# Performance work log

Hardware: AMD Instinct MI355X
Metric: run time of the kernel (lower is better)

## Reference

```python
import jax, jax.numpy as jnp
import numpy as np

N_HEADS = 16
N_KV_HEADS = 4
D_HEAD = 128
LN_EPS = 1e-5


def _layernorm_nobias(x, gamma):
    # LayerNorm over last dim, elementwise affine weight only (bias=False)
    mu = jnp.mean(x, axis=-1, keepdims=True)
    var = jnp.mean(jnp.square(x - mu), axis=-1, keepdims=True)
    return (x - mu) * jax.lax.rsqrt(var + LN_EPS) * gamma


def setup_inputs() -> dict:
    key = jax.random.key(0)
    ks = jax.random.split(key, 7)
    B, T, C = 1, 2048, 2048
    s = 1.0 / np.sqrt(C)
    return {
        "x": jax.random.normal(ks[0], (B, T, C), dtype=jnp.float32),
        "Wq": jax.random.normal(ks[1], (C, C), dtype=jnp.float32) * s,
        "Wk": jax.random.normal(ks[2], (C, N_KV_HEADS * D_HEAD), dtype=jnp.float32) * s,
        "Wv": jax.random.normal(ks[3], (C, N_KV_HEADS * D_HEAD), dtype=jnp.float32) * s,
        "Wo": jax.random.normal(ks[4], (C, C), dtype=jnp.float32) * s,
        "gq": jnp.ones((D_HEAD,), dtype=jnp.float32),
        "gk": jnp.ones((D_HEAD,), dtype=jnp.float32),
        "temp": jnp.asarray(np.log(10.0), dtype=jnp.float32),
    }


def reference(x, Wq, Wk, Wv, Wo, gq, gk, temp):
    B, T, C = x.shape
    g = N_HEADS // N_KV_HEADS
    q = (x @ Wq).reshape(B, T, N_HEADS, D_HEAD)
    k = (x @ Wk).reshape(B, T, N_KV_HEADS, D_HEAD)
    v = (x @ Wv).reshape(B, T, N_KV_HEADS, D_HEAD)
    # GQA: repeat_interleave kv heads along head dim
    k = jnp.repeat(k, g, axis=2)
    v = jnp.repeat(v, g, axis=2)
    q = _layernorm_nobias(q, gq)
    k = _layernorm_nobias(k, gk)
    scale = jnp.minimum(jnp.exp(temp), 50.0)
    scores = jnp.einsum('bthd,bshd->bhts', q, k) * scale  # [B,H,T,T]
    causal = jnp.tril(jnp.ones((T, T), dtype=bool))       # True = keep
    scores = jnp.where(causal[None, None], scores, -jnp.inf)
    attn = jax.nn.softmax(scores, axis=-1)
    out = jnp.einsum('bhts,bshd->bthd', attn, v).reshape(B, T, C)
    return out @ Wo
```

## Files before the change

### kernel.cpp

```cpp
#include <hip/hip_runtime.h>
#include <stdint.h>

typedef unsigned short u16;
typedef __bf16 bf16x8 __attribute__((ext_vector_type(8)));
typedef float f32x4 __attribute__((ext_vector_type(4)));
typedef float f32x2 __attribute__((ext_vector_type(2)));
typedef uint32_t u32x2 __attribute__((ext_vector_type(2)));
typedef uint32_t u32x4 __attribute__((ext_vector_type(4)));
typedef u16 u16x2 __attribute__((ext_vector_type(2)));

#define DEV static __device__ __forceinline__

constexpr int T = 2048;
constexpr int C = 2048;
constexpr int QKC = 2560;
constexpr int KVC = 512;

DEV u16 f2bf(float f) {
  union { float f; uint32_t u; } v; v.f = f;
  return (u16)((v.u + 0x7fffu + ((v.u >> 16) & 1u)) >> 16);
}
DEV float bf2f(u16 u) {
  union { uint32_t u; float f; } v; v.u = ((uint32_t)u) << 16;
  return v.f;
}

__global__ __launch_bounds__(256) void k_cvt2(const float* __restrict__ in,
                                              u16* __restrict__ oh,
                                              u16* __restrict__ ol, int n4) {
  int i = blockIdx.x * 256 + threadIdx.x;
  if (i >= n4) return;
  f32x4 f = ((const f32x4*)in)[i];
  u16 h[4], lo[4];
#pragma unroll
  for (int j = 0; j < 4; j++) {
    h[j] = f2bf(f[j]);
    lo[j] = f2bf(f[j] - bf2f(h[j]));
  }
  u32x2 ph, pl;
  ph.x = (uint32_t)h[0] | ((uint32_t)h[1] << 16);
  ph.y = (uint32_t)h[2] | ((uint32_t)h[3] << 16);
  pl.x = (uint32_t)lo[0] | ((uint32_t)lo[1] << 16);
  pl.y = (uint32_t)lo[2] | ((uint32_t)lo[3] << 16);
  ((u32x2*)oh)[i] = ph;
  ((u32x2*)ol)[i] = pl;
}

template <bool LO>
__global__ __launch_bounds__(256) void k_tcvt2(const float* __restrict__ in,
                                               u16* __restrict__ oh,
                                               u16* __restrict__ ol, int R, int Cc) {
  __shared__ u16 th[32][33];
  __shared__ u16 tl[32][33];
  int c0 = blockIdx.x * 32, r0 = blockIdx.y * 32;
  int tx = threadIdx.x, ty = threadIdx.y;
#pragma unroll
  for (int i = 0; i < 4; i++) {
    float f = in[(size_t)(r0 + ty + i * 8) * Cc + c0 + tx];
    u16 h = f2bf(f);
    th[ty + i * 8][tx] = h;
    if constexpr (LO) tl[ty + i * 8][tx] = f2bf(f - bf2f(h));
  }
  __syncthreads();
#pragma unroll
  for (int i = 0; i < 4; i++) {
    oh[(size_t)(c0 + ty + i * 8) * R + r0 + tx] = th[tx][ty + i * 8];
    if constexpr (LO)
      ol[(size_t)(c0 + ty + i * 8) * R + r0 + tx] = tl[tx][ty + i * 8];
  }
}

DEV void gload16(const u16* g, u16* lds) {
  __builtin_amdgcn_global_load_lds(
      (const __attribute__((address_space(1))) void*)g,
      (__attribute__((address_space(3))) void*)lds, 16, 0, 0);
}

__global__ __launch_bounds__(256) void k_gemmqkv(const u16* __restrict__ xh,
                                                 const u16* __restrict__ xl,
                                                 const u16* __restrict__ BTh,
                                                 const u16* __restrict__ BTl,
                                                 float* __restrict__ QKf,
                                                 u16* __restrict__ Vb) {
  __shared__ __align__(16) u16 As[128 * 32];
  __shared__ __align__(16) u16 Bs[128 * 32];
  const int tid = threadIdx.x;
  const int w = tid >> 6, l = tid & 63;
  const int m0 = blockIdx.y << 7, n0 = blockIdx.x << 7;
  const int wr = (w >> 1) * 64, wc = (w & 1) * 64;
  const int g = l >> 4, c = l & 15;
  const bool isV = (n0 >= 2560);
  const int nseg = isV ? 1 : 3;

  const size_t aoff = (size_t)(m0 + w * 32 + (l >> 2)) * C + (l & 3) * 8;
  const size_t boff = (size_t)(n0 + w * 32 + (l >> 2)) * C + (l & 3) * 8;
  u16* la = &As[(w * 32) * 32];
  u16* lb = &Bs[(w * 32) * 32];

  f32x4 acc[4][4] = {};

  for (int seg = 0; seg < nseg; ++seg) {
    const u16* ga = ((seg == 2) ? xl : xh) + aoff;
    const u16* gb = ((seg == 1) ? BTl : BTh) + boff;
    for (int k0 = 0; k0 < C; k0 += 32) {
      gload16(ga + k0, la);
      gload16(ga + k0 + 16 * C, la + 16 * 32);
      gload16(gb + k0, lb);
      gload16(gb + k0 + 16 * C, lb + 16 * 32);
      __syncthreads();
      bf16x8 af[4], bfr[4];
#pragma unroll
      for (int m = 0; m < 4; m++)
        af[m] = *(const bf16x8*)&As[(wr + m * 16 + c) * 32 + g * 8];
#pragma unroll
      for (int n = 0; n < 4; n++)
        bfr[n] = *(const bf16x8*)&Bs[(wc + n * 16 + c) * 32 + g * 8];
#pragma unroll
      for (int m = 0; m < 4; m++)
#pragma unroll
        for (int n = 0; n < 4; n++)
          acc[m][n] = __builtin_amdgcn_mfma_f32_16x16x32_bf16(af[m], bfr[n], acc[m][n], 0, 0, 0);
      __syncthreads();
    }
  }

#pragma unroll
  for (int m = 0; m < 4; m++) {
    int row = m0 + wr + m * 16 + g * 4;
#pragma unroll
    for (int n = 0; n < 4; n++) {
#pragma unroll
      for (int j = 0; j < 4; j++) {
        if (!isV) {
          int col = n0 + wc + n * 16 + c;
          QKf[(size_t)(row + j) * QKC + col] = acc[m][n][j];
        } else {
          int col = n0 - 2560 + wc + n * 16 + c;
          Vb[(size_t)(row + j) * KVC + col] = f2bf(acc[m][n][j]);
        }
      }
    }
  }
}

__global__ __launch_bounds__(256) void k_gemm(const u16* __restrict__ A,
                                              const u16* __restrict__ BT,
                                              float* __restrict__ Cout,
                                              int M, int N, int K) {
  __shared__ __align__(16) u16 As[128 * 32];
  __shared__ __align__(16) u16 Bs[128 * 32];
  const int tid = threadIdx.x;
  const int w = tid >> 6, l = tid & 63;
  const int m0 = blockIdx.y << 7, n0 = blockIdx.x << 7;
  const int wr = (w >> 1) * 64, wc = (w & 1) * 64;
  const int g = l >> 4, c = l & 15;

  f32x4 acc[4][4] = {};
  const u16* ga = A + (size_t)(m0 + w * 32 + (l >> 2)) * K + (l & 3) * 8;
  const u16* gb = BT + (size_t)(n0 + w * 32 + (l >> 2)) * K + (l & 3) * 8;
  u16* la = &As[(w * 32) * 32];
  u16* lb = &Bs[(w * 32) * 32];

  for (int k0 = 0; k0 < K; k0 += 32) {
    gload16(ga + k0, la);
    gload16(ga + k0 + (size_t)16 * K, la + 16 * 32);
    gload16(gb + k0, lb);
    gload16(gb + k0 + (size_t)16 * K, lb + 16 * 32);
    __syncthreads();
    bf16x8 af[4], bfr[4];
#pragma unroll
    for (int m = 0; m < 4; m++)
      af[m] = *(const bf16x8*)&As[(wr + m * 16 + c) * 32 + g * 8];
#pragma unroll
    for (int n = 0; n < 4; n++)
      bfr[n] = *(const bf16x8*)&Bs[(wc + n * 16 + c) * 32 + g * 8];
#pragma unroll
    for (int m = 0; m < 4; m++)
#pragma unroll
      for (int n = 0; n < 4; n++)
        acc[m][n] = __builtin_amdgcn_mfma_f32_16x16x32_bf16(af[m], bfr[n], acc[m][n], 0, 0, 0);
    __syncthreads();
  }

#pragma unroll
  for (int m = 0; m < 4; m++) {
    int row = m0 + wr + m * 16 + g * 4;
#pragma unroll
    for (int n = 0; n < 4; n++) {
      int col = n0 + wc + n * 16 + c;
#pragma unroll
      for (int j = 0; j < 4; j++)
        Cout[(size_t)(row + j) * N + col] = acc[m][n][j];
    }
  }
}

DEV void ln_row_f32(const float* __restrict__ x, const float* __restrict__ g,
                    u16* __restrict__ oh, u16* __restrict__ ol, int l) {
  f32x2 v = ((const f32x2*)x)[l];
  float s = v.x + v.y;
  float s2 = v.x * v.x + v.y * v.y;
#pragma unroll
  for (int m = 1; m < 64; m <<= 1) {
    s += __shfl_xor(s, m);
    s2 += __shfl_xor(s2, m);
  }
  float mu = s * (1.f / 128.f);
  float var = s2 * (1.f / 128.f) - mu * mu;
  float r = rsqrtf(var + 1e-5f);
  f32x2 gg = ((const f32x2*)g)[l];
  float y0 = (v.x - mu) * r * gg.x;
  float y1 = (v.y - mu) * r * gg.y;
  u16 h0 = f2bf(y0), h1 = f2bf(y1);
  u16x2 oh2, ol2;
  oh2.x = h0; oh2.y = h1;
  ol2.x = f2bf(y0 - bf2f(h0)); ol2.y = f2bf(y1 - bf2f(h1));
  ((u16x2*)oh)[l] = oh2;
  ((u16x2*)ol)[l] = ol2;
}

__global__ __launch_bounds__(256) void k_ln(const float* __restrict__ QKf,
                                            const float* __restrict__ gq,
                                            const float* __restrict__ gk,
                                            u16* __restrict__ Qh, u16* __restrict__ Ql,
                                            u16* __restrict__ Kh, u16* __restrict__ Kl) {
  int t = blockIdx.x;
  int w = threadIdx.x >> 6, l = threadIdx.x & 63;
  const float* row = QKf + (size_t)t * QKC;
#pragma unroll
  for (int i = 0; i < 4; i++) {
    int h = w * 4 + i;
    ln_row_f32(row + h * 128, gq, Qh + (size_t)t * C + h * 128,
               Ql + (size_t)t * C + h * 128, l);
  }
  ln_row_f32(row + 2048 + w * 128, gk, Kh + (size_t)t * KVC + w * 128,
             Kl + (size_t)t * KVC + w * 128, l);
}

__global__ __launch_bounds__(256) void k_attn(const u16* __restrict__ Qh_,
                                              const u16* __restrict__ Ql_,
                                              const u16* __restrict__ Kh_,
                                              const u16* __restrict__ Kl_,
                                              const u16* __restrict__ Vb,
                                              const float* __restrict__ temp,
                                              u16* __restrict__ Ob) {
  constexpr int VS = 40;
  __shared__ __align__(16) u16 Vt[128 * VS];
  __shared__ __align__(16) u16 Pl[4][16 * 32];
  const int h = blockIdx.y, kh = h >> 2;
  const int q0 = blockIdx.x << 6;
  const int tid = threadIdx.x;
  const int w = tid >> 6, l = tid & 63;
  const int g = l >> 4, c = l & 15;
  const float scale = fminf(expf(temp[0]), 50.f);

  bf16x8 qfh[4], qfl[4];
  {
    const size_t qo = (size_t)(q0 + w * 16 + c) * C + h * 128 + g * 8;
#pragma unroll
    for (int kk = 0; kk < 4; kk++) {
      qfh[kk] = *(const bf16x8*)(Qh_ + qo + kk * 32);
      qfl[kk] = *(const bf16x8*)(Ql_ + qo + kk * 32);
    }
  }

  f32x4 o[8] = {};
  float mi[4], li[4];
#pragma unroll
  for (int j = 0; j < 4; j++) { mi[j] = -INFINITY; li[j] = 0.f; }

  const int vs_s = tid & 31, vd0 = (tid >> 5) * 16;
  const int send = q0 + 64;
  for (int s0 = 0; s0 < send; s0 += 32) {
    __syncthreads();
    {
      const u16* vsrc = Vb + (size_t)(s0 + vs_s) * KVC + kh * 128 + vd0;
      u16 tmp[16];
      *(u32x4*)&tmp[0] = *(const u32x4*)vsrc;
      *(u32x4*)&tmp[8] = *(const u32x4*)(vsrc + 8);
#pragma unroll
      for (int j = 0; j < 16; j++) Vt[(vd0 + j) * VS + vs_s] = tmp[j];
    }
    __syncthreads();

    f32x4 sc[2] = {};
#pragma unroll
    for (int tile = 0; tile < 2; tile++) {
      const size_t ko = (size_t)(s0 + tile * 16 + c) * KVC + kh * 128 + g * 8;
#pragma unroll
      for (int kk = 0; kk < 4; kk++) {
        bf16x8 kfh = *(const bf16x8*)(Kh_ + ko + kk * 32);
        bf16x8 kfl = *(const bf16x8*)(Kl_ + ko + kk * 32);
        sc[tile] = __builtin_amdgcn_mfma_f32_16x16x32_bf16(qfh[kk], kfh, sc[tile], 0, 0, 0);
        sc[tile] = __builtin_amdgcn_mfma_f32_16x16x32_bf16(qfh[kk], kfl, sc[tile], 0, 0, 0);
        sc[tile] = __builtin_amdgcn_mfma_f32_16x16x32_bf16(qfl[kk], kfh, sc[tile], 0, 0, 0);
      }
    }

#pragma unroll
    for (int j = 0; j < 4; j++) {
      const int q = q0 + w * 16 + g * 4 + j;
      float x0 = sc[0][j] * scale; if (s0 + c > q) x0 = -INFINITY;
      float x1 = sc[1][j] * scale; if (s0 + 16 + c > q) x1 = -INFINITY;
      float mx = fmaxf(x0, x1);
#pragma unroll
      for (int msk = 1; msk < 16; msk <<= 1) mx = fmaxf(mx, __shfl_xor(mx, msk));
      float mn = fmaxf(mi[j], mx);
      float a = __expf(mi[j] - mn);
      float p0 = __expf(x0 - mn);
      float p1 = __expf(x1 - mn);
      float rs = p0 + p1;
#pragma unroll
      for (int msk = 1; msk < 16; msk <<= 1) rs += __shfl_xor(rs, msk);
      li[j] = li[j] * a + rs;
      mi[j] = mn;
#pragma unroll
      for (int dt = 0; dt < 8; dt++) o[dt][j] *= a;
      Pl[w][(g * 4 + j) * 32 + c] = f2bf(p0);
      Pl[w][(g * 4 + j) * 32 + 16 + c] = f2bf(p1);
    }

    bf16x8 pa = *(const bf16x8*)&Pl[w][c * 32 + g * 8];
#pragma unroll
    for (int dt = 0; dt < 8; dt++) {
      bf16x8 vf = *(const bf16x8*)&Vt[(dt * 16 + c) * VS + g * 8];
      o[dt] = __builtin_amdgcn_mfma_f32_16x16x32_bf16(pa, vf, o[dt], 0, 0, 0);
    }
  }

#pragma unroll
  for (int j = 0; j < 4; j++) {
    float inv = 1.f / li[j];
    u16* orow = Ob + (size_t)(q0 + w * 16 + g * 4 + j) * C + h * 128;
#pragma unroll
    for (int dt = 0; dt < 8; dt++) orow[dt * 16 + c] = f2bf(o[dt][j] * inv);
  }
}

extern "C" void kernel_launch(void* const* d_in, const int* in_sizes, int n_in,
                              void* d_out, int out_size, void* d_ws, size_t ws_size,
                              hipStream_t stream) {
  const float* x = (const float*)d_in[0];
  const float* Wq = (const float*)d_in[1];
  const float* Wk = (const float*)d_in[2];
  const float* Wv = (const float*)d_in[3];
  const float* Wo = (const float*)d_in[4];
  const float* gq = (const float*)d_in[5];
  const float* gk = (const float*)d_in[6];
  const float* temp = (const float*)d_in[7];
  float* out = (float*)d_out;

  constexpr size_t M1 = (size_t)1024 * 1024;
  u16* ws16 = (u16*)d_ws;
  u16* xh  = ws16;
  u16* xl  = xh + 4 * M1;
  u16* BTh = xl + 4 * M1;
  u16* BTl = BTh + 6 * M1;
  u16* WoT = BTl + 5 * M1;
  u16* Vb  = WoT + 4 * M1;
  float* QKf = (float*)(Vb + 1 * M1);
  u16* Qh = BTl;
  u16* Ql = BTh;
  u16* Kh = BTh + 4 * M1;
  u16* Kl = BTh + 5 * M1;
  u16* Ob = xh;

  k_cvt2<<<(T * C / 4 + 255) / 256, 256, 0, stream>>>(x, xh, xl, T * C / 4);
  k_tcvt2<true><<<dim3(C / 32, C / 32), dim3(32, 8), 0, stream>>>(Wq, BTh, BTl, C, C);
  k_tcvt2<true><<<dim3(KVC / 32, C / 32), dim3(32, 8), 0, stream>>>(
      Wk, BTh + (size_t)C * C, BTl + (size_t)C * C, C, KVC);
  k_tcvt2<false><<<dim3(KVC / 32, C / 32), dim3(32, 8), 0, stream>>>(
      Wv, BTh + (size_t)2560 * C, nullptr, C, KVC);
  k_tcvt2<false><<<dim3(C / 32, C / 32), dim3(32, 8), 0, stream>>>(Wo, WoT, nullptr, C, C);
  k_gemmqkv<<<dim3(3072 / 128, T / 128), 256, 0, stream>>>(xh, xl, BTh, BTl, QKf, Vb);
  k_ln<<<T, 256, 0, stream>>>(QKf, gq, gk, Qh, Ql, Kh, Kl);
  k_attn<<<dim3(T / 64, 16), 256, 0, stream>>>(Qh, Ql, Kh, Kl, Vb, temp, Ob);
  k_gemm<<<dim3(C / 128, T / 128), 256, 0, stream>>>(Ob, WoT, out, T, C, C);

  (void)in_sizes; (void)n_in; (void)out_size; (void)ws_size;
}
```

Before: 614.7 us.

## Fuse split-bf16 GEMM segments and widen attention tiles with row-sum via MFMA

The QKV GEMM now loads the hi and lo parts of A and B together and runs all three product terms in a single K loop instead of three separate passes. This reads the hi operands once rather than twice and removes two of the three loop restarts, at the cost of twice the LDS. The attention kernel uses 64-key tiles and register-prefetches the next V tile while the current one is processed. It also launches a flat grid ordered with the heaviest query tiles first, to balance the causal workload. The softmax row sum is no longer built from shuffle reductions; it comes from an extra MFMA against a ones column padded onto the V tile.

```diff
diff --git a/kernel.cpp b/kernel.cpp
--- a/kernel.cpp
+++ b/kernel.cpp
@@ -82,46 +82,71 @@
                                                  const u16* __restrict__ BTl,
                                                  float* __restrict__ QKf,
                                                  u16* __restrict__ Vb) {
-  __shared__ __align__(16) u16 As[128 * 32];
-  __shared__ __align__(16) u16 Bs[128 * 32];
+  __shared__ __align__(16) u16 Ahs[128 * 32];
+  __shared__ __align__(16) u16 Als[128 * 32];
+  __shared__ __align__(16) u16 Bhs[128 * 32];
+  __shared__ __align__(16) u16 Bls[128 * 32];
   const int tid = threadIdx.x;
   const int w = tid >> 6, l = tid & 63;
   const int m0 = blockIdx.y << 7, n0 = blockIdx.x << 7;
   const int wr = (w >> 1) * 64, wc = (w & 1) * 64;
   const int g = l >> 4, c = l & 15;
   const bool isV = (n0 >= 2560);
-  const int nseg = isV ? 1 : 3;
 
   const size_t aoff = (size_t)(m0 + w * 32 + (l >> 2)) * C + (l & 3) * 8;
   const size_t boff = (size_t)(n0 + w * 32 + (l >> 2)) * C + (l & 3) * 8;
-  u16* la = &As[(w * 32) * 32];
-  u16* lb = &Bs[(w * 32) * 32];
+  u16* lah = &Ahs[(w * 32) * 32];
+  u16* lal = &Als[(w * 32) * 32];
+  u16* lbh = &Bhs[(w * 32) * 32];
+  u16* lbl = &Bls[(w * 32) * 32];
 
   f32x4 acc[4][4] = {};
 
-  for (int seg = 0; seg < nseg; ++seg) {
-    const u16* ga = ((seg == 2) ? xl : xh) + aoff;
-    const u16* gb = ((seg == 1) ? BTl : BTh) + boff;
-    for (int k0 = 0; k0 < C; k0 += 32) {
-      gload16(ga + k0, la);
-      gload16(ga + k0 + 16 * C, la + 16 * 32);
-      gload16(gb + k0, lb);
-      gload16(gb + k0 + 16 * C, lb + 16 * 32);
-      __syncthreads();
-      bf16x8 af[4], bfr[4];
+  for (int k0 = 0; k0 < C; k0 += 32) {
+    gload16(xh + aoff + k0, lah);
+    gload16(xh + aoff + k0 + 16 * C, lah + 16 * 32);
+    gload16(BTh + boff + k0, lbh);
+    gload16(BTh + boff + k0 + 16 * C, lbh + 16 * 32);
+    if (!isV) {
+      gload16(xl + aoff + k0, lal);
+      gload16(xl + aoff + k0 + 16 * C, lal + 16 * 32);
+      gload16(BTl + boff + k0, lbl);
+      gload16(BTl + boff + k0 + 16 * C, lbl + 16 * 32);
+    }
+    __syncthreads();
+    bf16x8 afh[4], bfh[4];
+#pragma unroll
+    for (int m = 0; m < 4; m++)
+      afh[m] = *(const bf16x8*)&Ahs[(wr + m * 16 + c) * 32 + g * 8];
+#pragma unroll
+    for (int n = 0; n < 4; n++)
+      bfh[n] = *(const bf16x8*)&Bhs[(wc + n * 16 + c) * 32 + g * 8];
+#pragma unroll
+    for (int m = 0; m < 4; m++)
+#pragma unroll
+      for (int n = 0; n < 4; n++)
+        acc[m][n] = __builtin_amdgcn_mfma_f32_16x16x32_bf16(afh[m], bfh[n], acc[m][n], 0, 0, 0);
+    if (!isV) {
+      bf16x8 bfl[4];
+#pragma unroll
+      for (int n = 0; n < 4; n++)
+        bfl[n] = *(const bf16x8*)&Bls[(wc + n * 16 + c) * 32 + g * 8];
 #pragma unroll
       for (int m = 0; m < 4; m++)
-        af[m] = *(const bf16x8*)&As[(wr + m * 16 + c) * 32 + g * 8];
-#pragma unroll
-      for (int n = 0; n < 4; n++)
-        bfr[n] = *(const bf16x8*)&Bs[(wc + n * 16 + c) * 32 + g * 8];
+#pragma unroll
+        for (int n = 0; n < 4; n++)
+          acc[m][n] = __builtin_amdgcn_mfma_f32_16x16x32_bf16(afh[m], bfl[n], acc[m][n], 0, 0, 0);
+      bf16x8 afl[4];
 #pragma unroll
       for (int m = 0; m < 4; m++)
+        afl[m] = *(const bf16x8*)&Als[(wr + m * 16 + c) * 32 + g * 8];
+#pragma unroll
+      for (int m = 0; m < 4; m++)
 #pragma unroll
         for (int n = 0; n < 4; n++)
-          acc[m][n] = __builtin_amdgcn_mfma_f32_16x16x32_bf16(af[m], bfr[n], acc[m][n], 0, 0, 0);
-      __syncthreads();
-    }
+          acc[m][n] = __builtin_amdgcn_mfma_f32_16x16x32_bf16(afl[m], bfh[n], acc[m][n], 0, 0, 0);
+    }
+    __syncthreads();
   }
 
 #pragma unroll
@@ -244,15 +269,22 @@
                                               const u16* __restrict__ Vb,
                                               const float* __restrict__ temp,
                                               u16* __restrict__ Ob) {
-  constexpr int VS = 40;
-  __shared__ __align__(16) u16 Vt[128 * VS];
-  __shared__ __align__(16) u16 Pl[4][16 * 32];
-  const int h = blockIdx.y, kh = h >> 2;
-  const int q0 = blockIdx.x << 6;
+  constexpr int VS = 72;
+  __shared__ __align__(16) u16 Vt[144 * VS];
+  __shared__ __align__(16) u16 Pl[4][16 * VS];
+  const int flat = blockIdx.x;
+  const int qt = 31 - (flat >> 4);
+  const int h = flat & 15, kh = h >> 2;
+  const int q0 = qt << 6;
   const int tid = threadIdx.x;
   const int w = tid >> 6, l = tid & 63;
   const int g = l >> 4, c = l & 15;
-  const float scale = fminf(expf(temp[0]), 50.f);
+  const float scale = fminf(__expf(temp[0]), 50.f);
+
+  for (int idx = tid; idx < 16 * VS; idx += 256) {
+    int r = idx / VS, s = idx - r * VS;
+    Vt[(128 + r) * VS + s] = (r == 0 && s < 64) ? (u16)0x3F80 : (u16)0;
+  }
 
   bf16x8 qfh[4], qfl[4];
   {
@@ -265,75 +297,93 @@
   }
 
   f32x4 o[8] = {};
-  float mi[4], li[4];
-#pragma unroll
-  for (int j = 0; j < 4; j++) { mi[j] = -INFINITY; li[j] = 0.f; }
-
-  const int vs_s = tid & 31, vd0 = (tid >> 5) * 16;
-  const int send = q0 + 64;
-  for (int s0 = 0; s0 < send; s0 += 32) {
-    __syncthreads();
-    {
-      const u16* vsrc = Vb + (size_t)(s0 + vs_s) * KVC + kh * 128 + vd0;
-      u16 tmp[16];
-      *(u32x4*)&tmp[0] = *(const u32x4*)vsrc;
-      *(u32x4*)&tmp[8] = *(const u32x4*)(vsrc + 8);
-#pragma unroll
-      for (int j = 0; j < 16; j++) Vt[(vd0 + j) * VS + vs_s] = tmp[j];
-    }
-    __syncthreads();
-
-    f32x4 sc[2] = {};
-#pragma unroll
-    for (int tile = 0; tile < 2; tile++) {
-      const size_t ko = (size_t)(s0 + tile * 16 + c) * KVC + kh * 128 + g * 8;
-#pragma unroll
-      for (int kk = 0; kk < 4; kk++) {
+  f32x4 o2 = {0.f, 0.f, 0.f, 0.f};
+  float mi[4];
+#pragma unroll
+  for (int j = 0; j < 4; j++) mi[j] = -INFINITY;
+
+  const int vs_s = tid & 63, vd0 = (tid >> 6) * 32;
+  const int nit = qt + 1;
+
+  union { u32x4 v4[4]; u16 h16[32]; } vst;
+  {
+    const u16* vsrc = Vb + (size_t)vs_s * KVC + kh * 128 + vd0;
+    vst.v4[0] = *(const u32x4*)(vsrc);
+    vst.v4[1] = *(const u32x4*)(vsrc + 8);
+    vst.v4[2] = *(const u32x4*)(vsrc + 16);
+    vst.v4[3] = *(const u32x4*)(vsrc + 24);
+  }
+
+  for (int it = 0; it < nit; ++it) {
+    const int s0 = it << 6;
+    __syncthreads();
+#pragma unroll
+    for (int j = 0; j < 32; ++j) Vt[(vd0 + j) * VS + vs_s] = vst.h16[j];
+    __syncthreads();
+    if (it + 1 < nit) {
+      const u16* vsrc = Vb + (size_t)((it + 1) * 64 + vs_s) * KVC + kh * 128 + vd0;
+      vst.v4[0] = *(const u32x4*)(vsrc);
+      vst.v4[1] = *(const u32x4*)(vsrc + 8);
+      vst.v4[2] = *(const u32x4*)(vsrc + 16);
+      vst.v4[3] = *(const u32x4*)(vsrc + 24);
+    }
+
+    f32x4 sc[4] = {};
+#pragma unroll
+    for (int t = 0; t < 4; ++t) {
+      const size_t ko = (size_t)(s0 + t * 16 + c) * KVC + kh * 128 + g * 8;
+#pragma unroll
+      for (int kk = 0; kk < 4; ++kk) {
         bf16x8 kfh = *(const bf16x8*)(Kh_ + ko + kk * 32);
         bf16x8 kfl = *(const bf16x8*)(Kl_ + ko + kk * 32);
-        sc[tile] = __builtin_amdgcn_mfma_f32_16x16x32_bf16(qfh[kk], kfh, sc[tile], 0, 0, 0);
-        sc[tile] = __builtin_amdgcn_mfma_f32_16x16x32_bf16(qfh[kk], kfl, sc[tile], 0, 0, 0);
-        sc[tile] = __builtin_amdgcn_mfma_f32_16x16x32_bf16(qfl[kk], kfh, sc[tile], 0, 0, 0);
+        sc[t] = __builtin_amdgcn_mfma_f32_16x16x32_bf16(qfh[kk], kfh, sc[t], 0, 0, 0);
+        sc[t] = __builtin_amdgcn_mfma_f32_16x16x32_bf16(qfh[kk], kfl, sc[t], 0, 0, 0);
+        sc[t] = __builtin_amdgcn_mfma_f32_16x16x32_bf16(qfl[kk], kfh, sc[t], 0, 0, 0);
       }
     }
 
 #pragma unroll
-    for (int j = 0; j < 4; j++) {
+    for (int j = 0; j < 4; ++j) {
       const int q = q0 + w * 16 + g * 4 + j;
       float x0 = sc[0][j] * scale; if (s0 + c > q) x0 = -INFINITY;
       float x1 = sc[1][j] * scale; if (s0 + 16 + c > q) x1 = -INFINITY;
-      float mx = fmaxf(x0, x1);
+      float x2 = sc[2][j] * scale; if (s0 + 32 + c > q) x2 = -INFINITY;
+      float x3 = sc[3][j] * scale; if (s0 + 48 + c > q) x3 = -INFINITY;
+      float mx = fmaxf(fmaxf(x0, x1), fmaxf(x2, x3));
 #pragma unroll
       for (int msk = 1; msk < 16; msk <<= 1) mx = fmaxf(mx, __shfl_xor(mx, msk));
       float mn = fmaxf(mi[j], mx);
       float a = __expf(mi[j] - mn);
-      float p0 = __expf(x0 - mn);
-      float p1 = __expf(x1 - mn);
-      float rs = p0 + p1;
-#pragma unroll
-      for (int msk = 1; msk < 16; msk <<= 1) rs += __shfl_xor(rs, msk);
-      li[j] = li[j] * a + rs;
       mi[j] = mn;
 #pragma unroll
-      for (int dt = 0; dt < 8; dt++) o[dt][j] *= a;
-      Pl[w][(g * 4 + j) * 32 + c] = f2bf(p0);
-      Pl[w][(g * 4 + j) * 32 + 16 + c] = f2bf(p1);
-    }
-
-    bf16x8 pa = *(const bf16x8*)&Pl[w][c * 32 + g * 8];
-#pragma unroll
-    for (int dt = 0; dt < 8; dt++) {
-      bf16x8 vf = *(const bf16x8*)&Vt[(dt * 16 + c) * VS + g * 8];
-      o[dt] = __builtin_amdgcn_mfma_f32_16x16x32_bf16(pa, vf, o[dt], 0, 0, 0);
-    }
-  }
-
-#pragma unroll
-  for (int j = 0; j < 4; j++) {
-    float inv = 1.f / li[j];
+      for (int dt = 0; dt < 8; ++dt) o[dt][j] *= a;
+      o2[j] *= a;
+      Pl[w][(g * 4 + j) * VS + c]      = f2bf(__expf(x0 - mn));
+      Pl[w][(g * 4 + j) * VS + 16 + c] = f2bf(__expf(x1 - mn));
+      Pl[w][(g * 4 + j) * VS + 32 + c] = f2bf(__expf(x2 - mn));
+      Pl[w][(g * 4 + j) * VS + 48 + c] = f2bf(__expf(x3 - mn));
+    }
+
+#pragma unroll
+    for (int ks = 0; ks < 2; ++ks) {
+      bf16x8 pa = *(const bf16x8*)&Pl[w][c * VS + ks * 32 + g * 8];
+#pragma unroll
+      for (int dt = 0; dt < 8; ++dt) {
+        bf16x8 vf = *(const bf16x8*)&Vt[(dt * 16 + c) * VS + ks * 32 + g * 8];
+        o[dt] = __builtin_amdgcn_mfma_f32_16x16x32_bf16(pa, vf, o[dt], 0, 0, 0);
+      }
+      bf16x8 vo = *(const bf16x8*)&Vt[(128 + c) * VS + ks * 32 + g * 8];
+      o2 = __builtin_amdgcn_mfma_f32_16x16x32_bf16(pa, vo, o2, 0, 0, 0);
+    }
+  }
+
+#pragma unroll
+  for (int j = 0; j < 4; ++j) {
+    float li = __shfl(o2[j], l & 48);
+    float inv = 1.f / li;
     u16* orow = Ob + (size_t)(q0 + w * 16 + g * 4 + j) * C + h * 128;
 #pragma unroll
-    for (int dt = 0; dt < 8; dt++) orow[dt * 16 + c] = f2bf(o[dt][j] * inv);
+    for (int dt = 0; dt < 8; ++dt) orow[dt * 16 + c] = f2bf(o[dt][j] * inv);
   }
 }
 
@@ -374,7 +424,7 @@
   k_tcvt2<false><<<dim3(C / 32, C / 32), dim3(32, 8), 0, stream>>>(Wo, WoT, nullptr, C, C);
   k_gemmqkv<<<dim3(3072 / 128, T / 128), 256, 0, stream>>>(xh, xl, BTh, BTl, QKf, Vb);
   k_ln<<<T, 256, 0, stream>>>(QKf, gq, gk, Qh, Ql, Kh, Kl);
-  k_attn<<<dim3(T / 64, 16), 256, 0, stream>>>(Qh, Ql, Kh, Kl, Vb, temp, Ob);
+  k_attn<<<512, 256, 0, stream>>>(Qh, Ql, Kh, Kl, Vb, temp, Ob);
   k_gemm<<<dim3(C / 128, T / 128), 256, 0, stream>>>(Ob, WoT, out, T, C, C);
 
   (void)in_sizes; (void)n_in; (void)out_size; (void)ws_size;
```

New measurement: 497.2 us. 19.1% less time.
